# Kernel optimization log

Hardware: AMD Instinct MI355X
Metric: run time of the kernel (lower is better)

The kernel has to match this reference:

```python
import math
import jax, jax.numpy as jnp
import numpy as np

B, L, D, H, DFF, T, V = 512, 128, 128, 4, 256, 2048, 20000
LN_EPS = 1e-5
LOG_SIGMA0 = math.log(0.1)


def _keygen(base):
    c = [0]
    def nk():
        k = jax.random.fold_in(base, c[0]); c[0] += 1
        return k
    return nk


def bayes_linear(x, wmu, wls, bmu, bls, nk):
    # weight = mu + exp(log_sigma) * eps (fresh eps every call, as in BayesLinear.forward)
    w = wmu + jnp.exp(wls) * jax.random.normal(nk(), wmu.shape, wmu.dtype)
    b = bmu + jnp.exp(bls) * jax.random.normal(nk(), bmu.shape, bmu.dtype)
    return jnp.einsum('...d,od->...o', x, w) + b


def layer_norm(x, g, b):
    m = x.mean(-1, keepdims=True)
    v = ((x - m) ** 2).mean(-1, keepdims=True)
    return (x - m) / jnp.sqrt(v + LN_EPS) * g + b


def mha(q, k, v, wmu, wls, bmu, bls, nk):
    # wmu: [4, D, D] for q, k, v, o projections
    dk = D // H
    def proj(x, i):
        return bayes_linear(x, wmu[i], wls[i], bmu[i], bls[i], nk)
    def split(x):
        return x.reshape(B, L, H, dk).transpose(0, 2, 1, 3)
    Q, K, Vh = split(proj(q, 0)), split(proj(k, 1)), split(proj(v, 2))
    probs = jax.nn.softmax(jnp.einsum('bhqd,bhkd->bhqk', Q, K) / math.sqrt(dk), axis=-1)
    out = jnp.einsum('bhqk,bhkd->bhqd', probs, Vh).transpose(0, 2, 1, 3).reshape(B, L, D)
    return bayes_linear(out, wmu[3], wls[3], bmu[3], bls[3], nk)


def setup_inputs() -> dict:
    key = jax.random.key(0)
    ks = iter(jax.random.split(key, 64))
    def u(shape, fan_in):
        s = 1.0 / math.sqrt(fan_in)
        return jax.random.uniform(next(ks), shape, jnp.float32, -s, s)
    def ls(shape):
        return jnp.full(shape, LOG_SIGMA0, jnp.float32)
    return dict(
        event_set=jax.random.randint(next(ks), (B, L), 0, V),
        time=jax.random.uniform(next(ks), (B, L), jnp.float32),
        mask=jax.random.randint(next(ks), (B, L), 0, L),
        set_size=jax.random.randint(next(ks), (B,), 1, L),
        emb=jax.random.normal(next(ks), (V, D), jnp.float32),
        dec_wmu=u((2, 8, D, D), D), dec_wls=ls((2, 8, D, D)),
        dec_bmu=u((2, 8, D), D), dec_bls=ls((2, 8, D)),
        ffn1_wmu=u((2, DFF, D), D), ffn1_wls=ls((2, DFF, D)),
        ffn1_bmu=u((2, DFF), D), ffn1_bls=ls((2, DFF)),
        ffn2_wmu=u((2, D, DFF), DFF), ffn2_wls=ls((2, D, DFF)),
        ffn2_bmu=u((2, D), DFF), ffn2_bls=ls((2, D)),
        ln_g=jnp.ones((2, 3, D), jnp.float32), ln_b=jnp.zeros((2, 3, D), jnp.float32),
        alpha_wmu=u((5, T, D), D), alpha_wls=ls((5, T, D)),
        alpha_bmu=u((5, T), D), alpha_bls=ls((5, T)),
        at_wmu=u((5, 1, D), D), at_wls=ls((5, 1, D)),
        at_bmu=u((5, 1), D), at_bls=ls((5, 1)),
        em_w=u((5, T, D), D), em_b=u((5, T), D),
        es_w=u((5, T, D), D), es_b=u((5, T), D),
        tm_w=u((5, 1, D), D), tm_b=u((5, 1), D),
        ts_w=u((5, 1, D), D), ts_b=u((5, 1), D),
    )


def reference(event_set, time, mask, set_size, emb,
              dec_wmu, dec_wls, dec_bmu, dec_bls,
              ffn1_wmu, ffn1_wls, ffn1_bmu, ffn1_bls,
              ffn2_wmu, ffn2_wls, ffn2_bmu, ffn2_bls,
              ln_g, ln_b, alpha_wmu, alpha_wls, alpha_bmu, alpha_bls,
              at_wmu, at_wls, at_bmu, at_bls,
              em_w, em_b, es_w, es_b, tm_w, tm_b, ts_w, ts_b):
    nk = _keygen(jax.random.key(42))
    x = emb[event_set]                                     # [B, L, D]
    # sinusoidal positional encoding driven by `mask` (integer positions)
    pos = mask.astype(jnp.float32)
    div = jnp.exp(jnp.arange(D, dtype=jnp.float32) * (-math.log(10000.0) / D))
    ang = pos[..., None] * div                             # [B, L, D]
    pos_enc = jnp.where((mask % 2 == 0)[..., None], jnp.sin(ang), jnp.cos(ang))
    inp_x = x + pos_enc
    # two decoder layers: self-attn on x, cross-attn against inp_x (dropout = eval identity)
    for l in range(2):
        a = mha(x, x, x, dec_wmu[l, :4], dec_wls[l, :4], dec_bmu[l, :4], dec_bls[l, :4], nk)
        x = layer_norm(x + a, ln_g[l, 0], ln_b[l, 0])
        a = mha(x, inp_x, inp_x, dec_wmu[l, 4:], dec_wls[l, 4:], dec_bmu[l, 4:], dec_bls[l, 4:], nk)
        x = layer_norm(x + a, ln_g[l, 1], ln_b[l, 1])
        h1 = jax.nn.relu(bayes_linear(x, ffn1_wmu[l], ffn1_wls[l], ffn1_bmu[l], ffn1_bls[l], nk))
        f = bayes_linear(h1, ffn2_wmu[l], ffn2_wls[l], ffn2_bmu[l], ffn2_bls[l], nk)
        x = layer_norm(x + f, ln_g[l, 2], ln_b[l, 2])
    h = x[:, 0, :]                                          # [B, D]
    # 5 Bayesian alpha heads -> softmax over mixture dim (vectorized over k)
    aw = alpha_wmu + jnp.exp(alpha_wls) * jax.random.normal(nk(), alpha_wmu.shape)
    ab = alpha_bmu + jnp.exp(alpha_bls) * jax.random.normal(nk(), alpha_bmu.shape)
    alpha = jax.nn.softmax(jnp.einsum('bd,ktd->btk', h, aw) + ab.T[None], axis=2)   # [B, T, 5]
    atw = at_wmu + jnp.exp(at_wls) * jax.random.normal(nk(), at_wmu.shape)
    atb = at_bmu + jnp.exp(at_bls) * jax.random.normal(nk(), at_bmu.shape)
    alpha_t = jax.nn.softmax(jnp.einsum('bd,kd->bk', h, atw[:, 0]) + atb[:, 0][None], axis=1)  # [B, 5]
    # mixture of 5 reparameterized Gaussian predictors (plain Linears)
    means = jnp.einsum('bd,ktd->bkt', h, em_w) + em_b[None]          # [B, 5, T]
    stds = jnp.exp(jnp.einsum('bd,ktd->bkt', h, es_w) + es_b[None])
    noise_e = jax.random.normal(nk(), (B, 5, T))
    event_pred = jnp.sum(jnp.swapaxes(alpha, 1, 2) * (means + stds * noise_e), axis=1)   # [B, T]
    tmeans = jnp.einsum('bd,kd->bk', h, tm_w[:, 0]) + tm_b[:, 0][None]                   # [B, 5]
    tstds = jnp.exp(jnp.einsum('bd,kd->bk', h, ts_w[:, 0]) + ts_b[:, 0][None])
    noise_t = jax.random.normal(nk(), (B, 5))
    time_pred = jnp.sum(alpha_t * (tmeans + tstds * noise_t), axis=1, keepdims=True)     # [B, 1]
    return event_pred, time_pred
```

## Files before the change

### kernel.cpp

```cpp
#include <hip/hip_runtime.h>
#include <cstdint>
#include <cstddef>


#define NB   512
#define NL   128
#define ND   128
#define NH   4
#define NDFF 256
#define NT   2048
#define BL   (NB * NL)

typedef __attribute__((ext_vector_type(8))) short bf16x8;
typedef __attribute__((ext_vector_type(4))) float f32x4;

#define MFMA16(a, b, c) __builtin_amdgcn_mfma_f32_16x16x32_bf16((a), (b), (c), 0, 0, 0)

__host__ __device__ __forceinline__ void tf2x32(uint32_t k0, uint32_t k1,
                                                uint32_t x0, uint32_t x1,
                                                uint32_t& o0, uint32_t& o1)
{
  const uint32_t ks2 = k0 ^ k1 ^ 0x1BD11BDAu;
  x0 += k0; x1 += k1;
#define TF_RND(r) { x0 += x1; x1 = (x1 << (r)) | (x1 >> (32 - (r))); x1 ^= x0; }
  TF_RND(13) TF_RND(15) TF_RND(26) TF_RND(6)
  x0 += k1;  x1 += ks2 + 1u;
  TF_RND(17) TF_RND(29) TF_RND(16) TF_RND(24)
  x0 += ks2; x1 += k0 + 2u;
  TF_RND(13) TF_RND(15) TF_RND(26) TF_RND(6)
  x0 += k0;  x1 += k1 + 3u;
  TF_RND(17) TF_RND(29) TF_RND(16) TF_RND(24)
  x0 += k1;  x1 += ks2 + 4u;
  TF_RND(13) TF_RND(15) TF_RND(26) TF_RND(6)
  x0 += ks2; x1 += k0 + 5u;
#undef TF_RND
  o0 = x0; o1 = x1;
}

__device__ __forceinline__ float erfinv32(float x)
{
  float w = -log1pf(-__fmul_rn(x, x));
  float p;
  if (w < 5.0f) {
    w = w - 2.5f;
    p = 2.81022636e-08f;
    p = __fadd_rn( 3.43273939e-07f, __fmul_rn(p, w));
    p = __fadd_rn(-3.5233877e-06f,  __fmul_rn(p, w));
    p = __fadd_rn(-4.39150654e-06f, __fmul_rn(p, w));
    p = __fadd_rn( 0.00021858087f,  __fmul_rn(p, w));
    p = __fadd_rn(-0.00125372503f,  __fmul_rn(p, w));
    p = __fadd_rn(-0.00417768164f,  __fmul_rn(p, w));
    p = __fadd_rn( 0.246640727f,    __fmul_rn(p, w));
    p = __fadd_rn( 1.50140941f,     __fmul_rn(p, w));
  } else {
    w = sqrtf(w) - 3.0f;
    p = -0.000200214257f;
    p = __fadd_rn( 0.000100950558f, __fmul_rn(p, w));
    p = __fadd_rn( 0.00134934322f,  __fmul_rn(p, w));
    p = __fadd_rn(-0.00367342844f,  __fmul_rn(p, w));
    p = __fadd_rn( 0.00573950773f,  __fmul_rn(p, w));
    p = __fadd_rn(-0.0076224613f,   __fmul_rn(p, w));
    p = __fadd_rn( 0.00943887047f,  __fmul_rn(p, w));
    p = __fadd_rn( 1.00167406f,     __fmul_rn(p, w));
    p = __fadd_rn( 2.83297682f,     __fmul_rn(p, w));
  }
  return __fmul_rn(p, x);
}

__device__ __forceinline__ float bits_to_normal(uint32_t bits)
{
  const float lo = -0.99999994f;
  float f = __uint_as_float((bits >> 9) | 0x3F800000u) - 1.0f;
  float u = __fadd_rn(__fmul_rn(f, 2.0f), lo);
  u = fmaxf(lo, u);
  return __fmul_rn(1.41421356f, erfinv32(u));
}

__device__ __forceinline__ float jax_normal_idx(uint32_t k0, uint32_t k1, uint32_t idx)
{
  uint32_t o0, o1;
  tf2x32(k0, k1, 0u, idx, o0, o1);
  return bits_to_normal(o0 ^ o1);
}

__device__ __forceinline__ ushort f2bf(float f)
{
  uint32_t u = __float_as_uint(f);
  u += 0x7fffu + ((u >> 16) & 1u);
  return (ushort)(u >> 16);
}

__device__ __forceinline__ int pk128(int row, int col)
{
  return (((row >> 4) * 4 + (col >> 5)) * 64 + ((col >> 3) & 3) * 16 + (row & 15)) * 8
         + (col & 7);
}
__device__ __forceinline__ int pk_w2(int row, int col)
{
  return (col >> 7) * 16384 +
         (((row >> 4) * 4 + ((col >> 5) & 3)) * 64 + ((col >> 3) & 3) * 16 + (row & 15)) * 8
         + (col & 7);
}

__device__ __forceinline__ int swzc(int row, int chunk)
{
  return row * 128 + ((chunk ^ (row & 15)) << 3);
}
__device__ __forceinline__ int swz(int row, int col)
{
  return row * 128 + ((((col >> 3) ^ (row & 15)) << 3) | (col & 7));
}

#define SA_DECB 262144
#define SA_F1W  264192
#define SA_F1B  329728
#define SA_F2W  330240
#define SA_F2B  395776
#define SA_AW   396032
#define SA_AB   1706752
#define SA_ATW  1716992
#define SA_ATB  1717632
#define SA_TOT  1717637

#define BW_DEC  0
#define BW_F1   262144
#define BW_F2   327680
#define BW_AW   393216
#define BW_TOT  1703936

#define BF_DECB 0
#define BF_F1B  2048
#define BF_F2B  2560
#define BF_AB   2816
#define BF_ATW  13056
#define BF_ATB  13696
#define BF_TOT  13701

__global__ __launch_bounds__(256) void sample_all_kernel(
    const float* __restrict__ dec_wmu, const float* __restrict__ dec_wls,
    const float* __restrict__ dec_bmu, const float* __restrict__ dec_bls,
    const float* __restrict__ f1_wmu,  const float* __restrict__ f1_wls,
    const float* __restrict__ f1_bmu,  const float* __restrict__ f1_bls,
    const float* __restrict__ f2_wmu,  const float* __restrict__ f2_wls,
    const float* __restrict__ f2_bmu,  const float* __restrict__ f2_bls,
    const float* __restrict__ a_wmu,   const float* __restrict__ a_wls,
    const float* __restrict__ a_bmu,   const float* __restrict__ a_bls,
    const float* __restrict__ at_wmu,  const float* __restrict__ at_wls,
    const float* __restrict__ at_bmu,  const float* __restrict__ at_bls,
    ushort* __restrict__ wbf, float* __restrict__ wf32)
{
  const int i = blockIdx.x * 256 + threadIdx.x;
  if (i >= SA_TOT) return;
  const float* mu; const float* ls;
  uint32_t c, idx;
  int bf_dst = -1, f32_dst = -1;
  if (i < SA_DECB) {
    int s = i >> 14, t = i & 16383;
    mu = dec_wmu + i; ls = dec_wls + i;
    c = 2u * s + (s >= 8 ? 4u : 0u); idx = (uint32_t)t;
    bf_dst = BW_DEC + s * 16384 + pk128(t >> 7, t & 127);
  } else if (i < SA_F1W) {
    int t = i - SA_DECB; int s = t >> 7;
    mu = dec_bmu + t; ls = dec_bls + t;
    c = 2u * s + 1u + (s >= 8 ? 4u : 0u); idx = (uint32_t)(t & 127);
    f32_dst = BF_DECB + t;
  } else if (i < SA_F1B) {
    int t = i - SA_F1W; int s = t >> 15, tl = t & 32767;
    mu = f1_wmu + t; ls = f1_wls + t;
    c = 16u + 20u * s; idx = (uint32_t)tl;
    bf_dst = BW_F1 + s * 32768 + pk128(tl >> 7, tl & 127);
  } else if (i < SA_F2W) {
    int t = i - SA_F1B; int s = t >> 8;
    mu = f1_bmu + t; ls = f1_bls + t;
    c = 17u + 20u * s; idx = (uint32_t)(t & 255);
    f32_dst = BF_F1B + t;
  } else if (i < SA_F2B) {
    int t = i - SA_F2W; int s = t >> 15, tl = t & 32767;
    mu = f2_wmu + t; ls = f2_wls + t;
    c = 18u + 20u * s; idx = (uint32_t)tl;
    bf_dst = BW_F2 + s * 32768 + pk_w2(tl >> 8, tl & 255);
  } else if (i < SA_AW) {
    int t = i - SA_F2B; int s = t >> 7;
    mu = f2_bmu + t; ls = f2_bls + t;
    c = 19u + 20u * s; idx = (uint32_t)(t & 127);
    f32_dst = BF_F2B + t;
  } else if (i < SA_AB) {
    int t = i - SA_AW;
    mu = a_wmu + t; ls = a_wls + t; c = 40u; idx = (uint32_t)t;
    int kcomp = t >> 18, rem = t & 262143;
    bf_dst = BW_AW + pk128(kcomp * 2048 + (rem >> 7), rem & 127);
  } else if (i < SA_ATW) {
    int t = i - SA_AB;
    mu = a_bmu + t; ls = a_bls + t; c = 41u; idx = (uint32_t)t;
    f32_dst = BF_AB + t;
  } else if (i < SA_ATB) {
    int t = i - SA_ATW;
    mu = at_wmu + t; ls = at_wls + t; c = 42u; idx = (uint32_t)t;
    f32_dst = BF_ATW + t;
  } else {
    int t = i - SA_ATB;
    mu = at_bmu + t; ls = at_bls + t; c = 43u; idx = (uint32_t)t;
    f32_dst = BF_ATB + t;
  }
  uint32_t k0, k1;
  tf2x32(0u, 42u, 0u, c, k0, k1);
  float v = mu[0] + expf(ls[0]) * jax_normal_idx(k0, k1, idx);
  if (bf_dst >= 0) wbf[bf_dst] = f2bf(v);
  else             wf32[f32_dst] = v;
}

__global__ __launch_bounds__(256) void pack_head_kernel(
    const float* __restrict__ em_w, const float* __restrict__ es_w,
    ushort* __restrict__ EMp, ushort* __restrict__ ESp)
{
  int i = blockIdx.x * 256 + threadIdx.x;
  int kcomp = i >> 18, rem = i & 262143;
  int dst = pk128(kcomp * 2048 + (rem >> 7), rem & 127);
  EMp[dst] = f2bf(em_w[i]);
  ESp[dst] = f2bf(es_w[i]);
}

__global__ __launch_bounds__(512, 1) void decoder_mega_kernel(
    const int* __restrict__ ev, const int* __restrict__ mask,
    const float* __restrict__ emb,
    const ushort* __restrict__ WBF, const float* __restrict__ WF32,
    const float* __restrict__ lng_all, const float* __restrict__ lnb_all,
    float* __restrict__ Xh, ushort* __restrict__ Hb)
{
  __shared__ ushort WAu[16384];
  __shared__ ushort WBu[16384];
  __shared__ ushort KtU[16384];
  __shared__ ushort VtU[16384];
  __shared__ ushort XbU[16384];

  const int b = blockIdx.x;
  const int tid = threadIdx.x;
  const int w = tid >> 6, l = tid & 63;
  const int g = l >> 4, r16 = l & 15;
  const f32x4 zero = {0.f, 0.f, 0.f, 0.f};

  auto stageW = [&](ushort* dst, const ushort* src) {
#pragma unroll
    for (int it = 0; it < 4; ++it) {
      __builtin_amdgcn_global_load_lds(
          (const uint32_t*)(src + (size_t)(it * 512 + tid) * 8),
          (uint32_t*)(dst + (it * 512 + w * 64) * 8), 16, 0, 0);
    }
  };
  auto wfrag = [&](const ushort* WBp, int fid) -> bf16x8 {
    return *(const bf16x8*)(WBp + (size_t)((fid << 6) + l) * 8);
  };

  const ushort* firstW[6];
  firstW[0] = WBF + BW_DEC + (size_t)1 * 16384;
  firstW[1] = WBF + BW_DEC + (size_t)5 * 16384;
  firstW[2] = WBF + BW_F1;
  firstW[3] = WBF + BW_DEC + (size_t)9 * 16384;
  firstW[4] = WBF + BW_DEC + (size_t)13 * 16384;
  firstW[5] = WBF + BW_F1 + 32768;

  stageW(WAu, firstW[0]);

  float xreg[8][4];
  {
    int ecr[4];
#pragma unroll
    for (int r = 0; r < 4; ++r) ecr[r] = ev[b * NL + 16 * w + 4 * g + r];
#pragma unroll
    for (int c = 0; c < 8; ++c)
#pragma unroll
      for (int r = 0; r < 4; ++r) {
        float x = emb[(size_t)ecr[r] * ND + 16 * c + r16];
        xreg[c][r] = x;
        XbU[swz(16 * w + 4 * g + r, 16 * c + r16)] = f2bf(x);
      }
  }
  bf16x8 inpx[4];
  {
    const int row = 16 * w + r16;
    const int ea = ev[b * NL + row];
    const int mk = mask[b * NL + row];
    const bool even = (mk & 1) == 0;
    const float fm = (float)mk;
#pragma unroll
    for (int ks = 0; ks < 4; ++ks) {
      float4 x0 = *(const float4*)(emb + (size_t)ea * ND + 32 * ks + 8 * g);
      float4 x1 = *(const float4*)(emb + (size_t)ea * ND + 32 * ks + 8 * g + 4);
      float xs[8] = {x0.x, x0.y, x0.z, x0.w, x1.x, x1.y, x1.z, x1.w};
      bf16x8 v;
#pragma unroll
      for (int e = 0; e < 8; ++e) {
        int d = 32 * ks + 8 * g + e;
        float div = expf((float)d * (float)(-9.210340371976184 / 128.0));
        float ang = fm * div;
        float pe = even ? sinf(ang) : cosf(ang);
        v[e] = (short)f2bf(xs[e] + pe);
      }
      inpx[ks] = v;
    }
  }

#pragma unroll 1
  for (int st = 0; st < 6; ++st) {
    const int lay = st / 3, m = st - 3 * lay;
    const float* lng = lng_all + (size_t)(lay * 3 + m) * ND;
    const float* lnb = lnb_all + (size_t)(lay * 3 + m) * ND;
    f32x4 acc2[8];
#pragma unroll
    for (int c = 0; c < 8; ++c) acc2[c] = zero;
    float bo[8];

    if (m < 2) {
      const int s0 = lay * 8 + m * 4;
      const ushort* Wq = WBF + BW_DEC + (size_t)(s0 + 0) * 16384;
      const ushort* Wv = WBF + BW_DEC + (size_t)(s0 + 2) * 16384;
      const ushort* Wo = WBF + BW_DEC + (size_t)(s0 + 3) * 16384;
      const float*  B4 = WF32 + BF_DECB + (size_t)s0 * 128;

      __syncthreads();
      stageW(WBu, Wv);
      f32x4 kacc[8];
#pragma unroll
      for (int c = 0; c < 8; ++c) kacc[c] = zero;
#pragma unroll
      for (int ks = 0; ks < 4; ++ks) {
        bf16x8 a = (m == 0) ? *(const bf16x8*)&XbU[swzc(16 * w + r16, 4 * ks + g)]
                            : inpx[ks];
#pragma unroll
        for (int c = 0; c < 8; ++c)
          kacc[c] = MFMA16(a, wfrag(WAu, 4 * c + ks), kacc[c]);
      }

      __syncthreads();
      stageW(WAu, Wq);
#pragma unroll
      for (int c = 0; c < 8; ++c) {
        float kb = B4[128 + 16 * c + r16];
#pragma unroll
        for (int r = 0; r < 4; ++r)
          KtU[swz(16 * w + 4 * g + r, 16 * c + r16)] = f2bf(kacc[c][r] + kb);
      }
      {
        f32x4 vacc[8];
#pragma unroll
        for (int c = 0; c < 8; ++c) vacc[c] = zero;
#pragma unroll
        for (int ks = 0; ks < 4; ++ks) {
          bf16x8 a = (m == 0) ? *(const bf16x8*)&XbU[swzc(16 * w + r16, 4 * ks + g)]
                              : inpx[ks];
#pragma unroll
          for (int c = 0; c < 8; ++c)
            vacc[c] = MFMA16(a, wfrag(WBu, 4 * c + ks), vacc[c]);
        }
#pragma unroll
        for (int c = 0; c < 8; ++c) {
          float vb = B4[256 + 16 * c + r16];
          ushort4 pkv;
          pkv.x = f2bf(vacc[c][0] + vb); pkv.y = f2bf(vacc[c][1] + vb);
          pkv.z = f2bf(vacc[c][2] + vb); pkv.w = f2bf(vacc[c][3] + vb);
          *(ushort4*)&VtU[swzc(16 * c + r16, 2 * w + (g >> 1)) + (g & 1) * 4] = pkv;
        }
      }

      __syncthreads();
      stageW(WBu, Wo);
      {
        f32x4 qacc[8];
#pragma unroll
        for (int c = 0; c < 8; ++c) qacc[c] = zero;
#pragma unroll
        for (int ks = 0; ks < 4; ++ks) {
          bf16x8 a = *(const bf16x8*)&XbU[swzc(16 * w + r16, 4 * ks + g)];
#pragma unroll
          for (int c = 0; c < 8; ++c)
            qacc[c] = MFMA16(a, wfrag(WAu, 4 * c + ks), qacc[c]);
        }
#pragma unroll
        for (int c = 0; c < 8; ++c) {
          float qb = B4[16 * c + r16];
#pragma unroll
          for (int r = 0; r < 4; ++r)
            XbU[swz(16 * w + 4 * g + r, 16 * c + r16)] = f2bf(qacc[c][r] + qb);
        }
      }

      __syncthreads();
      ushort (*Ps)[72] = (ushort(*)[72])WAu;
      const float scale = 0.1767766952966369f;
      f32x4 oacc[4][2];
#pragma unroll
      for (int h = 0; h < 4; ++h) { oacc[h][0] = zero; oacc[h][1] = zero; }
#pragma unroll
      for (int h = 0; h < 4; ++h) {
        bf16x8 qa = *(const bf16x8*)&XbU[swzc(16 * w + r16, 4 * h + g)];
        f32x4 s[8];
#pragma unroll
        for (int c = 0; c < 8; ++c) {
          bf16x8 kv = *(const bf16x8*)&KtU[swzc(16 * c + r16, 4 * h + g)];
          s[c] = MFMA16(qa, kv, zero);
        }
        float pv[4][8];
#pragma unroll
        for (int r = 0; r < 4; ++r) {
          float v[8]; float mx = -1e30f;
#pragma unroll
          for (int c = 0; c < 8; ++c) { v[c] = s[c][r] * scale; mx = fmaxf(mx, v[c]); }
#pragma unroll
          for (int o = 1; o < 16; o <<= 1) mx = fmaxf(mx, __shfl_xor(mx, o));
          float sum = 0.f;
#pragma unroll
          for (int c = 0; c < 8; ++c) { v[c] = __expf(v[c] - mx); sum += v[c]; }
#pragma unroll
          for (int o = 1; o < 16; o <<= 1) sum += __shfl_xor(sum, o);
          float inv = 1.0f / sum;
#pragma unroll
          for (int c = 0; c < 8; ++c) pv[r][c] = v[c] * inv;
        }
#pragma unroll
        for (int kc = 0; kc < 4; ++kc) {
          const int po = (kc & 1) * 32;
#pragma unroll
          for (int c2 = 0; c2 < 2; ++c2)
#pragma unroll
            for (int r = 0; r < 4; ++r)
              Ps[16 * w + 4 * g + r][po + 16 * c2 + r16] = f2bf(pv[r][2 * kc + c2]);
          bf16x8 pa = *(const bf16x8*)&Ps[16 * w + r16][po + 8 * g];
#pragma unroll
          for (int cc = 0; cc < 2; ++cc) {
            bf16x8 vv = *(const bf16x8*)&VtU[swzc(32 * h + 16 * cc + r16, 4 * kc + g)];
            oacc[h][cc] = MFMA16(pa, vv, oacc[h][cc]);
          }
        }
      }

      __syncthreads();
      if (st < 5) stageW(WAu, firstW[st + 1]);
#pragma unroll
      for (int h = 0; h < 4; ++h)
#pragma unroll
        for (int cc = 0; cc < 2; ++cc)
#pragma unroll
          for (int r = 0; r < 4; ++r)
            KtU[swz(16 * w + 4 * g + r, 32 * h + 16 * cc + r16)] = f2bf(oacc[h][cc][r]);
#pragma unroll
      for (int ks = 0; ks < 4; ++ks) {
        bf16x8 a = *(const bf16x8*)&KtU[swzc(16 * w + r16, 4 * ks + g)];
#pragma unroll
        for (int c = 0; c < 8; ++c)
          acc2[c] = MFMA16(a, wfrag(WBu, 4 * c + ks), acc2[c]);
      }
#pragma unroll
      for (int c = 0; c < 8; ++c) bo[c] = B4[384 + 16 * c + r16];
    } else {
      const ushort* W1p = WBF + BW_F1 + (size_t)lay * 32768;
      const ushort* W2p = WBF + BW_F2 + (size_t)lay * 32768;
      const float*  B1 = WF32 + BF_F1B + (size_t)lay * 256;
      const float*  B2 = WF32 + BF_F2B + (size_t)lay * 128;

      __syncthreads();
      stageW(WBu, W1p + 16384);
      f32x4 acc1a[8];
#pragma unroll
      for (int c = 0; c < 8; ++c) acc1a[c] = zero;
#pragma unroll
      for (int ks = 0; ks < 4; ++ks) {
        bf16x8 a = *(const bf16x8*)&XbU[swzc(16 * w + r16, 4 * ks + g)];
#pragma unroll
        for (int c = 0; c < 8; ++c)
          acc1a[c] = MFMA16(a, wfrag(WAu, 4 * c + ks), acc1a[c]);
      }

      __syncthreads();
      stageW(WAu, W2p);
      {
        f32x4 acc1b[8];
#pragma unroll
        for (int c = 0; c < 8; ++c) acc1b[c] = zero;
#pragma unroll
        for (int ks = 0; ks < 4; ++ks) {
          bf16x8 a = *(const bf16x8*)&XbU[swzc(16 * w + r16, 4 * ks + g)];
#pragma unroll
          for (int c = 0; c < 8; ++c)
            acc1b[c] = MFMA16(a, wfrag(WBu, 4 * c + ks), acc1b[c]);
        }
#pragma unroll
        for (int c = 0; c < 8; ++c) {
          float b1a = B1[16 * c + r16];
#pragma unroll
          for (int r = 0; r < 4; ++r)
            VtU[swz(16 * w + 4 * g + r, 16 * c + r16)] =
                f2bf(fmaxf(acc1a[c][r] + b1a, 0.f));
          float b1b = B1[128 + 16 * c + r16];
#pragma unroll
          for (int r = 0; r < 4; ++r)
            KtU[swz(16 * w + 4 * g + r, 16 * c + r16)] =
                f2bf(fmaxf(acc1b[c][r] + b1b, 0.f));
        }
      }

      __syncthreads();
      stageW(WBu, W2p + 16384);
#pragma unroll
      for (int kl = 0; kl < 4; ++kl) {
        bf16x8 a = *(const bf16x8*)&VtU[swzc(16 * w + r16, 4 * kl + g)];
#pragma unroll
        for (int c = 0; c < 8; ++c)
          acc2[c] = MFMA16(a, wfrag(WAu, 4 * c + kl), acc2[c]);
      }

      __syncthreads();
      if (st < 5) stageW(WAu, firstW[st + 1]);
#pragma unroll
      for (int kl = 0; kl < 4; ++kl) {
        bf16x8 a = *(const bf16x8*)&KtU[swzc(16 * w + r16, 4 * kl + g)];
#pragma unroll
        for (int c = 0; c < 8; ++c)
          acc2[c] = MFMA16(a, wfrag(WBu, 4 * c + kl), acc2[c]);
      }
#pragma unroll
      for (int c = 0; c < 8; ++c) bo[c] = B2[16 * c + r16];
    }

    float gg[8], lb[8];
#pragma unroll
    for (int c = 0; c < 8; ++c) { gg[c] = lng[16 * c + r16]; lb[c] = lnb[16 * c + r16]; }
#pragma unroll
    for (int r = 0; r < 4; ++r) {
      float xv[8];
#pragma unroll
      for (int c = 0; c < 8; ++c) xv[c] = acc2[c][r] + bo[c] + xreg[c][r];
      float s = 0.f;
#pragma unroll
      for (int c = 0; c < 8; ++c) s += xv[c];
#pragma unroll
      for (int o = 1; o < 16; o <<= 1) s += __shfl_xor(s, o);
      float mean = s * (1.0f / 128.0f);
      float q = 0.f;
#pragma unroll
      for (int c = 0; c < 8; ++c) { float d = xv[c] - mean; q += d * d; }
#pragma unroll
      for (int o = 1; o < 16; o <<= 1) q += __shfl_xor(q, o);
      float inv = 1.0f / sqrtf(q * (1.0f / 128.0f) + 1e-5f);
#pragma unroll
      for (int c = 0; c < 8; ++c) {
        float o = (xv[c] - mean) * inv * gg[c] + lb[c];
        xreg[c][r] = o;
        XbU[swz(16 * w + 4 * g + r, 16 * c + r16)] = f2bf(o);
      }
    }
  }

  if (w == 0 && g == 0) {
#pragma unroll
    for (int c = 0; c < 8; ++c) {
      Xh[(size_t)b * ND + 16 * c + r16] = xreg[c][0];
      Hb[(size_t)b * ND + 16 * c + r16] = f2bf(xreg[c][0]);
    }
  }
}

__global__ __launch_bounds__(256) void head_fused_kernel(
    const ushort* __restrict__ Hb,
    const ushort* __restrict__ AWp, const float* __restrict__ ABs,
    const ushort* __restrict__ EMp, const float* __restrict__ em_b,
    const ushort* __restrict__ ESp, const float* __restrict__ es_b,
    float* __restrict__ out, uint32_t k0, uint32_t k1)
{
  const int tt = blockIdx.x;
  const int t0 = tt * 16;
  const int bm = blockIdx.y * 128;
  const int tid = threadIdx.x;
  const int w = tid >> 6, l = tid & 63;
  const int g = l >> 4, r16 = l & 15;
  const f32x4 zero = {0.f, 0.f, 0.f, 0.f};
  const int tl = t0 + r16;

  f32x4 aA[2][5], aE[2][5], aS[2][5];
#pragma unroll
  for (int t = 0; t < 2; ++t)
#pragma unroll
    for (int k = 0; k < 5; ++k) { aA[t][k] = zero; aE[t][k] = zero; aS[t][k] = zero; }

#pragma unroll
  for (int ks = 0; ks < 4; ++ks) {
    bf16x8 a0 = *(const bf16x8*)(Hb + (size_t)(bm + 32 * w + r16) * 128 + 32 * ks + 8 * g);
    bf16x8 a1 = *(const bf16x8*)(Hb + (size_t)(bm + 32 * w + 16 + r16) * 128 + 32 * ks + 8 * g);
#pragma unroll
    for (int k = 0; k < 5; ++k) {
      const size_t CB = (((size_t)(k * 128 + tt) * 4 + ks) * 64 + l) * 8;
      bf16x8 wa = *(const bf16x8*)(AWp + CB);
      aA[0][k] = MFMA16(a0, wa, aA[0][k]);
      aA[1][k] = MFMA16(a1, wa, aA[1][k]);
      bf16x8 we = *(const bf16x8*)(EMp + CB);
      aE[0][k] = MFMA16(a0, we, aE[0][k]);
      aE[1][k] = MFMA16(a1, we, aE[1][k]);
      bf16x8 wsv = *(const bf16x8*)(ESp + CB);
      aS[0][k] = MFMA16(a0, wsv, aS[0][k]);
      aS[1][k] = MFMA16(a1, wsv, aS[1][k]);
    }
  }

  float bA[5], bE[5], bS[5];
#pragma unroll
  for (int k = 0; k < 5; ++k) {
    bA[k] = ABs[k * NT + tl];
    bE[k] = em_b[k * NT + tl];
    bS[k] = es_b[k * NT + tl];
  }

#pragma unroll
  for (int t = 0; t < 2; ++t)
#pragma unroll
    for (int r = 0; r < 4; ++r) {
      const int brow = bm + 32 * w + 16 * t + 4 * g + r;
      float lg[5];
      float mx = -1e30f;
#pragma unroll
      for (int k = 0; k < 5; ++k) { lg[k] = aA[t][k][r] + bA[k]; mx = fmaxf(mx, lg[k]); }
      float se = 0.f;
#pragma unroll
      for (int k = 0; k < 5; ++k) { lg[k] = expf(lg[k] - mx); se += lg[k]; }
      const float inv = 1.0f / se;
      float acc = 0.f;
#pragma unroll
      for (int k = 0; k < 5; ++k) {
        float nz = jax_normal_idx(k0, k1, (uint32_t)((brow * 5 + k) * NT + tl));
        float mean = aE[t][k][r] + bE[k];
        float sd   = expf(aS[t][k][r] + bS[k]);
        acc += (lg[k] * inv) * (mean + sd * nz);
      }
      out[(size_t)brow * NT + tl] = acc;
    }
}

__global__ __launch_bounds__(64) void time_head_kernel(
    const float* __restrict__ Xh, const float* __restrict__ atw,
    const float* __restrict__ atb, const float* __restrict__ tmw,
    const float* __restrict__ tmb, const float* __restrict__ tsw,
    const float* __restrict__ tsb, float* __restrict__ out,
    uint32_t k0, uint32_t k1)
{
  const int b = blockIdx.x;
  const int l = threadIdx.x;
  const float* h = Xh + (size_t)b * ND;
  const float h0 = h[l], h1 = h[l + 64];
  float lg[5], tm[5], tsl[5];
#pragma unroll
  for (int k = 0; k < 5; ++k) {
    float s0 = fmaf(h0, atw[k * ND + l], h1 * atw[k * ND + l + 64]);
    float s1 = fmaf(h0, tmw[k * ND + l], h1 * tmw[k * ND + l + 64]);
    float s2 = fmaf(h0, tsw[k * ND + l], h1 * tsw[k * ND + l + 64]);
#pragma unroll
    for (int o = 32; o; o >>= 1) {
      s0 += __shfl_xor(s0, o);
      s1 += __shfl_xor(s1, o);
      s2 += __shfl_xor(s2, o);
    }
    lg[k] = s0 + atb[k]; tm[k] = s1 + tmb[k]; tsl[k] = s2 + tsb[k];
  }
  if (l == 0) {
    float mx = lg[0];
    for (int k = 1; k < 5; ++k) mx = fmaxf(mx, lg[k]);
    float se = 0.f;
    for (int k = 0; k < 5; ++k) { lg[k] = expf(lg[k] - mx); se += lg[k]; }
    float acc = 0.f;
    for (int k = 0; k < 5; ++k) {
      float nz = jax_normal_idx(k0, k1, (uint32_t)(b * 5 + k));
      acc += (lg[k] / se) * (tm[k] + expf(tsl[k]) * nz);
    }
    out[b] = acc;
  }
}

extern "C" void kernel_launch(void* const* d_in, const int* in_sizes, int n_in,
                              void* d_out, int out_size, void* d_ws, size_t ws_size,
                              hipStream_t stream)
{
  (void)in_sizes; (void)n_in; (void)out_size; (void)ws_size;

  const int*   ev      = (const int*)d_in[0];
  const int*   mask    = (const int*)d_in[2];
  const float* emb     = (const float*)d_in[4];
  const float* dec_wmu = (const float*)d_in[5];
  const float* dec_wls = (const float*)d_in[6];
  const float* dec_bmu = (const float*)d_in[7];
  const float* dec_bls = (const float*)d_in[8];
  const float* f1_wmu  = (const float*)d_in[9];
  const float* f1_wls  = (const float*)d_in[10];
  const float* f1_bmu  = (const float*)d_in[11];
  const float* f1_bls  = (const float*)d_in[12];
  const float* f2_wmu  = (const float*)d_in[13];
  const float* f2_wls  = (const float*)d_in[14];
  const float* f2_bmu  = (const float*)d_in[15];
  const float* f2_bls  = (const float*)d_in[16];
  const float* ln_g    = (const float*)d_in[17];
  const float* ln_b    = (const float*)d_in[18];
  const float* a_wmu   = (const float*)d_in[19];
  const float* a_wls   = (const float*)d_in[20];
  const float* a_bmu   = (const float*)d_in[21];
  const float* a_bls   = (const float*)d_in[22];
  const float* at_wmu  = (const float*)d_in[23];
  const float* at_wls  = (const float*)d_in[24];
  const float* at_bmu  = (const float*)d_in[25];
  const float* at_bls  = (const float*)d_in[26];
  const float* em_w    = (const float*)d_in[27];
  const float* em_b    = (const float*)d_in[28];
  const float* es_w    = (const float*)d_in[29];
  const float* es_b    = (const float*)d_in[30];
  const float* tm_w    = (const float*)d_in[31];
  const float* tm_b    = (const float*)d_in[32];
  const float* ts_w    = (const float*)d_in[33];
  const float* ts_b    = (const float*)d_in[34];

  float* ws = (float*)d_ws;
  ushort* WBF  = (ushort*)ws;
  float*  WF32 = ws + BW_TOT / 2;
  ushort* EMp  = (ushort*)(WF32 + BF_TOT + 3);
  ushort* ESp  = EMp + 5 * NT * ND;
  ushort* Hb   = ESp + 5 * NT * ND;
  float*  Xh   = (float*)(Hb + (size_t)NB * ND);

  uint32_t fk0[46], fk1[46];
  for (uint32_t c = 0; c < 46; ++c) tf2x32(0u, 42u, 0u, c, fk0[c], fk1[c]);

  sample_all_kernel<<<dim3((SA_TOT + 255) / 256), dim3(256), 0, stream>>>(
      dec_wmu, dec_wls, dec_bmu, dec_bls,
      f1_wmu, f1_wls, f1_bmu, f1_bls,
      f2_wmu, f2_wls, f2_bmu, f2_bls,
      a_wmu, a_wls, a_bmu, a_bls,
      at_wmu, at_wls, at_bmu, at_bls, WBF, WF32);

  pack_head_kernel<<<dim3((5 * NT * ND) / 256), dim3(256), 0, stream>>>(
      em_w, es_w, EMp, ESp);

  decoder_mega_kernel<<<dim3(NB), dim3(512), 0, stream>>>(
      ev, mask, emb, WBF, WF32, ln_g, ln_b, Xh, Hb);

  float* out = (float*)d_out;
  head_fused_kernel<<<dim3(NT / 16, 4), dim3(256), 0, stream>>>(
      Hb, WBF + BW_AW, WF32 + BF_AB, EMp, em_b, ESp, es_b,
      out, fk0[44], fk1[44]);
  time_head_kernel<<<dim3(NB), dim3(64), 0, stream>>>(
      Xh, WF32 + BF_ATW, WF32 + BF_ATB, tm_w, tm_b, ts_w, ts_b,
      out + (size_t)NB * NT, fk0[45], fk1[45]);
}
```

Measured before the change: 343.8 us.

## Hold decoder weight fragments in registers and split GEMMs by output column per wave

The decoder mega-kernel no longer stages each weight matrix into LDS through global_load_lds. Each wave now owns a 16-column slice of the output and keeps its weight fragments in registers, looping over all 128 rows of activations from LDS. Because the wave-to-column mapping changes, LayerNorm now reduces partial sums and sums of squares across waves through a small LDS buffer (one-pass variance), and the attention probabilities reuse XbU instead of a separate padded buffer. This removes the weight staging traffic and some barriers. In exchange it adds more LDS activation reads, extra synchronisations for LayerNorm, and more register pressure, and the one-pass variance can be less accurate.

Measured after the change: 621.5 us. 80.8% more time.

```diff
diff --git a/kernel.cpp b/kernel.cpp
--- a/kernel.cpp
+++ b/kernel.cpp
@@ -227,55 +227,38 @@
     const float* __restrict__ lng_all, const float* __restrict__ lnb_all,
     float* __restrict__ Xh, ushort* __restrict__ Hb)
 {
-  __shared__ ushort WAu[16384];
-  __shared__ ushort WBu[16384];
+  __shared__ ushort XbU[16384];
   __shared__ ushort KtU[16384];
   __shared__ ushort VtU[16384];
-  __shared__ ushort XbU[16384];
+  __shared__ ushort IxU[16384];
+  __shared__ float  LNs[2688];
+
+  float* Pp = LNs;
+  float* Pq = LNs + 1152;
+  float2* Mv = (float2*)(LNs + 2304);
 
   const int b = blockIdx.x;
   const int tid = threadIdx.x;
   const int w = tid >> 6, l = tid & 63;
   const int g = l >> 4, r16 = l & 15;
+  const int col = 16 * w + r16;
   const f32x4 zero = {0.f, 0.f, 0.f, 0.f};
 
-  auto stageW = [&](ushort* dst, const ushort* src) {
-#pragma unroll
-    for (int it = 0; it < 4; ++it) {
-      __builtin_amdgcn_global_load_lds(
-          (const uint32_t*)(src + (size_t)(it * 512 + tid) * 8),
-          (uint32_t*)(dst + (it * 512 + w * 64) * 8), 16, 0, 0);
+  auto ldfrag = [&](const ushort* Wp, int fid) -> bf16x8 {
+    return *(const bf16x8*)(Wp + ((size_t)(fid << 6) + l) * 8);
+  };
+
+  float xreg[8][4];
+#pragma unroll
+  for (int m8 = 0; m8 < 8; ++m8)
+#pragma unroll
+    for (int r = 0; r < 4; ++r) {
+      const int row = 16 * m8 + 4 * g + r;
+      const int e = ev[b * NL + row];
+      float x = emb[(size_t)e * ND + col];
+      xreg[m8][r] = x;
+      XbU[swz(row, col)] = f2bf(x);
     }
-  };
-  auto wfrag = [&](const ushort* WBp, int fid) -> bf16x8 {
-    return *(const bf16x8*)(WBp + (size_t)((fid << 6) + l) * 8);
-  };
-
-  const ushort* firstW[6];
-  firstW[0] = WBF + BW_DEC + (size_t)1 * 16384;
-  firstW[1] = WBF + BW_DEC + (size_t)5 * 16384;
-  firstW[2] = WBF + BW_F1;
-  firstW[3] = WBF + BW_DEC + (size_t)9 * 16384;
-  firstW[4] = WBF + BW_DEC + (size_t)13 * 16384;
-  firstW[5] = WBF + BW_F1 + 32768;
-
-  stageW(WAu, firstW[0]);
-
-  float xreg[8][4];
-  {
-    int ecr[4];
-#pragma unroll
-    for (int r = 0; r < 4; ++r) ecr[r] = ev[b * NL + 16 * w + 4 * g + r];
-#pragma unroll
-    for (int c = 0; c < 8; ++c)
-#pragma unroll
-      for (int r = 0; r < 4; ++r) {
-        float x = emb[(size_t)ecr[r] * ND + 16 * c + r16];
-        xreg[c][r] = x;
-        XbU[swz(16 * w + 4 * g + r, 16 * c + r16)] = f2bf(x);
-      }
-  }
-  bf16x8 inpx[4];
   {
     const int row = 16 * w + r16;
     const int ea = ev[b * NL + row];
@@ -296,9 +279,10 @@
         float pe = even ? sinf(ang) : cosf(ang);
         v[e] = (short)f2bf(xs[e] + pe);
       }
-      inpx[ks] = v;
+      *(bf16x8*)&IxU[swzc(row, 4 * ks + g)] = v;
     }
   }
+  __syncthreads();
 
 #pragma unroll 1
   for (int st = 0; st < 6; ++st) {
@@ -308,98 +292,101 @@
     f32x4 acc2[8];
 #pragma unroll
     for (int c = 0; c < 8; ++c) acc2[c] = zero;
-    float bo[8];
+    float bo_s;
 
     if (m < 2) {
       const int s0 = lay * 8 + m * 4;
       const ushort* Wq = WBF + BW_DEC + (size_t)(s0 + 0) * 16384;
+      const ushort* Wk = WBF + BW_DEC + (size_t)(s0 + 1) * 16384;
       const ushort* Wv = WBF + BW_DEC + (size_t)(s0 + 2) * 16384;
       const ushort* Wo = WBF + BW_DEC + (size_t)(s0 + 3) * 16384;
       const float*  B4 = WF32 + BF_DECB + (size_t)s0 * 128;
 
-      __syncthreads();
-      stageW(WBu, Wv);
-      f32x4 kacc[8];
-#pragma unroll
-      for (int c = 0; c < 8; ++c) kacc[c] = zero;
+      bf16x8 wk[4], wv[4], wq[4];
 #pragma unroll
       for (int ks = 0; ks < 4; ++ks) {
-        bf16x8 a = (m == 0) ? *(const bf16x8*)&XbU[swzc(16 * w + r16, 4 * ks + g)]
-                            : inpx[ks];
-#pragma unroll
-        for (int c = 0; c < 8; ++c)
-          kacc[c] = MFMA16(a, wfrag(WAu, 4 * c + ks), kacc[c]);
-      }
-
-      __syncthreads();
-      stageW(WAu, Wq);
-#pragma unroll
-      for (int c = 0; c < 8; ++c) {
-        float kb = B4[128 + 16 * c + r16];
-#pragma unroll
-        for (int r = 0; r < 4; ++r)
-          KtU[swz(16 * w + 4 * g + r, 16 * c + r16)] = f2bf(kacc[c][r] + kb);
+        wk[ks] = ldfrag(Wk, 4 * w + ks);
+        wv[ks] = ldfrag(Wv, 4 * w + ks);
+        wq[ks] = ldfrag(Wq, 4 * w + ks);
+      }
+      const ushort* Asrc = (m == 0) ? XbU : IxU;
+
+      {
+        f32x4 kacc[8];
+#pragma unroll
+        for (int c = 0; c < 8; ++c) kacc[c] = zero;
+#pragma unroll
+        for (int m8 = 0; m8 < 8; ++m8)
+#pragma unroll
+          for (int ks = 0; ks < 4; ++ks) {
+            bf16x8 a = *(const bf16x8*)&Asrc[swzc(16 * m8 + r16, 4 * ks + g)];
+            kacc[m8] = MFMA16(a, wk[ks], kacc[m8]);
+          }
+        float kb = B4[128 + col];
+#pragma unroll
+        for (int m8 = 0; m8 < 8; ++m8)
+#pragma unroll
+          for (int r = 0; r < 4; ++r)
+            KtU[swz(16 * m8 + 4 * g + r, col)] = f2bf(kacc[m8][r] + kb);
       }
       {
         f32x4 vacc[8];
 #pragma unroll
         for (int c = 0; c < 8; ++c) vacc[c] = zero;
 #pragma unroll
+        for (int m8 = 0; m8 < 8; ++m8)
+#pragma unroll
+          for (int ks = 0; ks < 4; ++ks) {
+            bf16x8 a = *(const bf16x8*)&Asrc[swzc(16 * m8 + r16, 4 * ks + g)];
+            vacc[m8] = MFMA16(a, wv[ks], vacc[m8]);
+          }
+        float vb = B4[256 + col];
+#pragma unroll
+        for (int m8 = 0; m8 < 8; ++m8) {
+          ushort4 pkv;
+          pkv.x = f2bf(vacc[m8][0] + vb); pkv.y = f2bf(vacc[m8][1] + vb);
+          pkv.z = f2bf(vacc[m8][2] + vb); pkv.w = f2bf(vacc[m8][3] + vb);
+          *(ushort4*)&VtU[swz(col, 16 * m8 + 4 * g)] = pkv;
+        }
+      }
+      f32x4 qacc[8];
+#pragma unroll
+      for (int c = 0; c < 8; ++c) qacc[c] = zero;
+#pragma unroll
+      for (int m8 = 0; m8 < 8; ++m8)
+#pragma unroll
         for (int ks = 0; ks < 4; ++ks) {
-          bf16x8 a = (m == 0) ? *(const bf16x8*)&XbU[swzc(16 * w + r16, 4 * ks + g)]
-                              : inpx[ks];
-#pragma unroll
-          for (int c = 0; c < 8; ++c)
-            vacc[c] = MFMA16(a, wfrag(WBu, 4 * c + ks), vacc[c]);
-        }
-#pragma unroll
-        for (int c = 0; c < 8; ++c) {
-          float vb = B4[256 + 16 * c + r16];
-          ushort4 pkv;
-          pkv.x = f2bf(vacc[c][0] + vb); pkv.y = f2bf(vacc[c][1] + vb);
-          pkv.z = f2bf(vacc[c][2] + vb); pkv.w = f2bf(vacc[c][3] + vb);
-          *(ushort4*)&VtU[swzc(16 * c + r16, 2 * w + (g >> 1)) + (g & 1) * 4] = pkv;
-        }
-      }
-
+          bf16x8 a = *(const bf16x8*)&XbU[swzc(16 * m8 + r16, 4 * ks + g)];
+          qacc[m8] = MFMA16(a, wq[ks], qacc[m8]);
+        }
       __syncthreads();
-      stageW(WBu, Wo);
       {
-        f32x4 qacc[8];
-#pragma unroll
-        for (int c = 0; c < 8; ++c) qacc[c] = zero;
-#pragma unroll
-        for (int ks = 0; ks < 4; ++ks) {
-          bf16x8 a = *(const bf16x8*)&XbU[swzc(16 * w + r16, 4 * ks + g)];
-#pragma unroll
-          for (int c = 0; c < 8; ++c)
-            qacc[c] = MFMA16(a, wfrag(WAu, 4 * c + ks), qacc[c]);
-        }
-#pragma unroll
-        for (int c = 0; c < 8; ++c) {
-          float qb = B4[16 * c + r16];
+        float qb = B4[col];
+#pragma unroll
+        for (int m8 = 0; m8 < 8; ++m8)
 #pragma unroll
           for (int r = 0; r < 4; ++r)
-            XbU[swz(16 * w + 4 * g + r, 16 * c + r16)] = f2bf(qacc[c][r] + qb);
-        }
-      }
-
+            XbU[swz(16 * m8 + 4 * g + r, col)] = f2bf(qacc[m8][r] + qb);
+      }
       __syncthreads();
-      ushort (*Ps)[72] = (ushort(*)[72])WAu;
+
+      bf16x8 qa[4];
+#pragma unroll
+      for (int h = 0; h < 4; ++h)
+        qa[h] = *(const bf16x8*)&XbU[swzc(16 * w + r16, 4 * h + g)];
+
       const float scale = 0.1767766952966369f;
       f32x4 oacc[4][2];
 #pragma unroll
       for (int h = 0; h < 4; ++h) { oacc[h][0] = zero; oacc[h][1] = zero; }
 #pragma unroll
       for (int h = 0; h < 4; ++h) {
-        bf16x8 qa = *(const bf16x8*)&XbU[swzc(16 * w + r16, 4 * h + g)];
         f32x4 s[8];
 #pragma unroll
         for (int c = 0; c < 8; ++c) {
           bf16x8 kv = *(const bf16x8*)&KtU[swzc(16 * c + r16, 4 * h + g)];
-          s[c] = MFMA16(qa, kv, zero);
-        }
-        float pv[4][8];
+          s[c] = MFMA16(qa[h], kv, zero);
+        }
 #pragma unroll
         for (int r = 0; r < 4; ++r) {
           float v[8]; float mx = -1e30f;
@@ -413,18 +400,14 @@
 #pragma unroll
           for (int o = 1; o < 16; o <<= 1) sum += __shfl_xor(sum, o);
           float inv = 1.0f / sum;
-#pragma unroll
-          for (int c = 0; c < 8; ++c) pv[r][c] = v[c] * inv;
+          const int prow = 16 * w + 4 * g + r;
+#pragma unroll
+          for (int c = 0; c < 8; ++c)
+            XbU[swz(prow, 16 * c + r16)] = f2bf(v[c] * inv);
         }
 #pragma unroll
         for (int kc = 0; kc < 4; ++kc) {
-          const int po = (kc & 1) * 32;
-#pragma unroll
-          for (int c2 = 0; c2 < 2; ++c2)
-#pragma unroll
-            for (int r = 0; r < 4; ++r)
-              Ps[16 * w + 4 * g + r][po + 16 * c2 + r16] = f2bf(pv[r][2 * kc + c2]);
-          bf16x8 pa = *(const bf16x8*)&Ps[16 * w + r16][po + 8 * g];
+          bf16x8 pa = *(const bf16x8*)&XbU[swzc(16 * w + r16, 4 * kc + g)];
 #pragma unroll
           for (int cc = 0; cc < 2; ++cc) {
             bf16x8 vv = *(const bf16x8*)&VtU[swzc(32 * h + 16 * cc + r16, 4 * kc + g)];
@@ -432,9 +415,11 @@
           }
         }
       }
-
       __syncthreads();
-      if (st < 5) stageW(WAu, firstW[st + 1]);
+
+      bf16x8 wo[4];
+#pragma unroll
+      for (int ks = 0; ks < 4; ++ks) wo[ks] = ldfrag(Wo, 4 * w + ks);
 #pragma unroll
       for (int h = 0; h < 4; ++h)
 #pragma unroll
@@ -442,120 +427,118 @@
 #pragma unroll
           for (int r = 0; r < 4; ++r)
             KtU[swz(16 * w + 4 * g + r, 32 * h + 16 * cc + r16)] = f2bf(oacc[h][cc][r]);
-#pragma unroll
-      for (int ks = 0; ks < 4; ++ks) {
-        bf16x8 a = *(const bf16x8*)&KtU[swzc(16 * w + r16, 4 * ks + g)];
-#pragma unroll
-        for (int c = 0; c < 8; ++c)
-          acc2[c] = MFMA16(a, wfrag(WBu, 4 * c + ks), acc2[c]);
-      }
-#pragma unroll
-      for (int c = 0; c < 8; ++c) bo[c] = B4[384 + 16 * c + r16];
+      __syncthreads();
+
+#pragma unroll
+      for (int m8 = 0; m8 < 8; ++m8)
+#pragma unroll
+        for (int ks = 0; ks < 4; ++ks) {
+          bf16x8 a = *(const bf16x8*)&KtU[swzc(16 * m8 + r16, 4 * ks + g)];
+          acc2[m8] = MFMA16(a, wo[ks], acc2[m8]);
+        }
+      bo_s = B4[384 + col];
     } else {
       const ushort* W1p = WBF + BW_F1 + (size_t)lay * 32768;
       const ushort* W2p = WBF + BW_F2 + (size_t)lay * 32768;
       const float*  B1 = WF32 + BF_F1B + (size_t)lay * 256;
       const float*  B2 = WF32 + BF_F2B + (size_t)lay * 128;
 
+#pragma unroll
+      for (int t = 0; t < 2; ++t) {
+        const int cblk = 2 * w + t;
+        bf16x8 w1[4];
+#pragma unroll
+        for (int ks = 0; ks < 4; ++ks) w1[ks] = ldfrag(W1p, 4 * cblk + ks);
+        f32x4 a1[8];
+#pragma unroll
+        for (int c = 0; c < 8; ++c) a1[c] = zero;
+#pragma unroll
+        for (int m8 = 0; m8 < 8; ++m8)
+#pragma unroll
+          for (int ks = 0; ks < 4; ++ks) {
+            bf16x8 a = *(const bf16x8*)&XbU[swzc(16 * m8 + r16, 4 * ks + g)];
+            a1[m8] = MFMA16(a, w1[ks], a1[m8]);
+          }
+        const int hcol = 32 * w + 16 * t + r16;
+        const float b1 = B1[hcol];
+        if (cblk < 8) {
+#pragma unroll
+          for (int m8 = 0; m8 < 8; ++m8)
+#pragma unroll
+            for (int r = 0; r < 4; ++r)
+              VtU[swz(16 * m8 + 4 * g + r, hcol)] = f2bf(fmaxf(a1[m8][r] + b1, 0.f));
+        } else {
+#pragma unroll
+          for (int m8 = 0; m8 < 8; ++m8)
+#pragma unroll
+            for (int r = 0; r < 4; ++r)
+              KtU[swz(16 * m8 + 4 * g + r, hcol - 128)] = f2bf(fmaxf(a1[m8][r] + b1, 0.f));
+        }
+      }
+      bf16x8 w2[8];
+#pragma unroll
+      for (int ks8 = 0; ks8 < 8; ++ks8)
+        w2[ks8] = ldfrag(W2p + (ks8 >= 4 ? 16384 : 0), 4 * w + (ks8 & 3));
       __syncthreads();
-      stageW(WBu, W1p + 16384);
-      f32x4 acc1a[8];
-#pragma unroll
-      for (int c = 0; c < 8; ++c) acc1a[c] = zero;
-#pragma unroll
-      for (int ks = 0; ks < 4; ++ks) {
-        bf16x8 a = *(const bf16x8*)&XbU[swzc(16 * w + r16, 4 * ks + g)];
-#pragma unroll
-        for (int c = 0; c < 8; ++c)
-          acc1a[c] = MFMA16(a, wfrag(WAu, 4 * c + ks), acc1a[c]);
-      }
-
-      __syncthreads();
-      stageW(WAu, W2p);
-      {
-        f32x4 acc1b[8];
-#pragma unroll
-        for (int c = 0; c < 8; ++c) acc1b[c] = zero;
-#pragma unroll
-        for (int ks = 0; ks < 4; ++ks) {
-          bf16x8 a = *(const bf16x8*)&XbU[swzc(16 * w + r16, 4 * ks + g)];
-#pragma unroll
-          for (int c = 0; c < 8; ++c)
-            acc1b[c] = MFMA16(a, wfrag(WBu, 4 * c + ks), acc1b[c]);
-        }
-#pragma unroll
-        for (int c = 0; c < 8; ++c) {
-          float b1a = B1[16 * c + r16];
-#pragma unroll
-          for (int r = 0; r < 4; ++r)
-            VtU[swz(16 * w + 4 * g + r, 16 * c + r16)] =
-                f2bf(fmaxf(acc1a[c][r] + b1a, 0.f));
-          float b1b = B1[128 + 16 * c + r16];
-#pragma unroll
-          for (int r = 0; r < 4; ++r)
-            KtU[swz(16 * w + 4 * g + r, 16 * c + r16)] =
-                f2bf(fmaxf(acc1b[c][r] + b1b, 0.f));
-        }
-      }
-
-      __syncthreads();
-      stageW(WBu, W2p + 16384);
-#pragma unroll
-      for (int kl = 0; kl < 4; ++kl) {
-        bf16x8 a = *(const bf16x8*)&VtU[swzc(16 * w + r16, 4 * kl + g)];
-#pragma unroll
-        for (int c = 0; c < 8; ++c)
-          acc2[c] = MFMA16(a, wfrag(WAu, 4 * c + kl), acc2[c]);
-      }
-
-      __syncthreads();
-      if (st < 5) stageW(WAu, firstW[st + 1]);
-#pragma unroll
-      for (int kl = 0; kl < 4; ++kl) {
-        bf16x8 a = *(const bf16x8*)&KtU[swzc(16 * w + r16, 4 * kl + g)];
-#pragma unroll
-        for (int c = 0; c < 8; ++c)
-          acc2[c] = MFMA16(a, wfrag(WBu, 4 * c + kl), acc2[c]);
-      }
-#pragma unroll
-      for (int c = 0; c < 8; ++c) bo[c] = B2[16 * c + r16];
+
+#pragma unroll
+      for (int m8 = 0; m8 < 8; ++m8)
+#pragma unroll
+        for (int ks8 = 0; ks8 < 8; ++ks8) {
+          bf16x8 a = (ks8 < 4)
+            ? *(const bf16x8*)&VtU[swzc(16 * m8 + r16, 4 * ks8 + g)]
+            : *(const bf16x8*)&KtU[swzc(16 * m8 + r16, 4 * (ks8 - 4) + g)];
+          acc2[m8] = MFMA16(a, w2[ks8], acc2[m8]);
+        }
+      bo_s = B2[col];
     }
 
-    float gg[8], lb[8];
-#pragma unroll
-    for (int c = 0; c < 8; ++c) { gg[c] = lng[16 * c + r16]; lb[c] = lnb[16 * c + r16]; }
-#pragma unroll
-    for (int r = 0; r < 4; ++r) {
-      float xv[8];
-#pragma unroll
-      for (int c = 0; c < 8; ++c) xv[c] = acc2[c][r] + bo[c] + xreg[c][r];
-      float s = 0.f;
-#pragma unroll
-      for (int c = 0; c < 8; ++c) s += xv[c];
-#pragma unroll
-      for (int o = 1; o < 16; o <<= 1) s += __shfl_xor(s, o);
+    const float gg = lng[col], lb = lnb[col];
+    float xv[8][4];
+#pragma unroll
+    for (int m8 = 0; m8 < 8; ++m8)
+#pragma unroll
+      for (int r = 0; r < 4; ++r)
+        xv[m8][r] = acc2[m8][r] + bo_s + xreg[m8][r];
+#pragma unroll
+    for (int m8 = 0; m8 < 8; ++m8)
+#pragma unroll
+      for (int r = 0; r < 4; ++r) {
+        float s = xv[m8][r], q = s * s;
+#pragma unroll
+        for (int o = 1; o < 16; o <<= 1) { s += __shfl_xor(s, o); q += __shfl_xor(q, o); }
+        if (r16 == 0) {
+          const int row = 16 * m8 + 4 * g + r;
+          Pp[row * 9 + w] = s;
+          Pq[row * 9 + w] = q;
+        }
+      }
+    __syncthreads();
+    if (tid < 128) {
+      float s = 0.f, q = 0.f;
+#pragma unroll
+      for (int u = 0; u < 8; ++u) { s += Pp[tid * 9 + u]; q += Pq[tid * 9 + u]; }
       float mean = s * (1.0f / 128.0f);
-      float q = 0.f;
-#pragma unroll
-      for (int c = 0; c < 8; ++c) { float d = xv[c] - mean; q += d * d; }
-#pragma unroll
-      for (int o = 1; o < 16; o <<= 1) q += __shfl_xor(q, o);
-      float inv = 1.0f / sqrtf(q * (1.0f / 128.0f) + 1e-5f);
-#pragma unroll
-      for (int c = 0; c < 8; ++c) {
-        float o = (xv[c] - mean) * inv * gg[c] + lb[c];
-        xreg[c][r] = o;
-        XbU[swz(16 * w + 4 * g + r, 16 * c + r16)] = f2bf(o);
-      }
+      float var = q * (1.0f / 128.0f) - mean * mean;
+      Mv[tid] = float2{mean, 1.0f / sqrtf(var + 1e-5f)};
     }
-  }
-
-  if (w == 0 && g == 0) {
-#pragma unroll
-    for (int c = 0; c < 8; ++c) {
-      Xh[(size_t)b * ND + 16 * c + r16] = xreg[c][0];
-      Hb[(size_t)b * ND + 16 * c + r16] = f2bf(xreg[c][0]);
-    }
+    __syncthreads();
+#pragma unroll
+    for (int m8 = 0; m8 < 8; ++m8)
+#pragma unroll
+      for (int r = 0; r < 4; ++r) {
+        const int row = 16 * m8 + 4 * g + r;
+        float2 mv = Mv[row];
+        float o = (xv[m8][r] - mv.x) * mv.y * gg + lb;
+        xreg[m8][r] = o;
+        XbU[swz(row, col)] = f2bf(o);
+      }
+    __syncthreads();
+  }
+
+  if (g == 0) {
+    Xh[(size_t)b * ND + col] = xreg[0][0];
+    Hb[(size_t)b * ND + col] = f2bf(xreg[0][0]);
   }
 }
 
```
